# Optimization experiments

Hardware: AMD Instinct MI355X
Metric: run time of the kernel (lower is better)

Reference implementation:

```python
import jax, jax.numpy as jnp
import numpy as np

N, C, E = 10000, 128, 640000  # nodes, channels, edges


def setup_inputs() -> dict:
    key = jax.random.key(0)
    k1, k2, k3, k4 = jax.random.split(key, 4)
    x = jax.random.normal(k1, (N, C), dtype=jnp.float32)
    src = jax.random.randint(k2, (E,), 0, N)  # source node of each edge (neighbor j)
    dst = jax.random.randint(k3, (E,), 0, N)  # destination node (center i)
    # EdgeConv linear: in = 2*C (concat[x_i, x_j - x_i]), out = C
    W = jax.random.normal(k4, (2 * C, C), dtype=jnp.float32) / np.sqrt(2.0 * C)
    b = jnp.zeros((C,), dtype=jnp.float32)
    return {"x": x, "W": W, "b": b, "src": src, "dst": dst}


def reference(x, W, b, src, dst):
    # EdgeConv: h_i = max_{j in N(i)} Linear([x_i, x_j - x_i]); then ReLU
    xi = x[dst]                                   # [E, C] gather center feats
    xj = x[src]                                   # [E, C] gather neighbor feats
    msg = jnp.concatenate([xi, xj - xi], axis=-1) @ W + b   # [E, C]
    agg = jax.ops.segment_max(msg, dst, num_segments=x.shape[0])  # [N, C]
    # nodes with no incoming edges get -inf from segment_max; zero them
    agg = jnp.where(jnp.isfinite(agg), agg, jnp.zeros_like(agg))
    return jax.nn.relu(agg)
```

## Files before the change

### kernel.cpp

```cpp
#include <hip/hip_runtime.h>
#include <cstdint>


#define C_CH 128
#define HBLK 256
#define BSH 4
#define BPAD 640

typedef __attribute__((ext_vector_type(8))) short bf16x8;
typedef __attribute__((ext_vector_type(4))) float f32x4;

static inline size_t align_up(size_t v, size_t a) { return (v + a - 1) & ~(a - 1); }

__device__ inline unsigned f2bf_bits(float f) {
    unsigned u = __builtin_bit_cast(unsigned, f);
    return (u + 0x7FFFu + ((u >> 16) & 1u)) >> 16;
}
__device__ inline unsigned mono_key(unsigned u) {
    return (u & 0x80000000u) ? ~u : (u | 0x80000000u);
}

__global__ __launch_bounds__(256) void gemm_mfma(const float* __restrict__ x,
                                                 const float* __restrict__ W,
                                                 const float* __restrict__ bias,
                                                 float* __restrict__ Aarr,
                                                 unsigned short* __restrict__ Bbf,
                                                 int Nn) {
    __shared__ unsigned short Wh[64][136];
    __shared__ unsigned short Wl[64][136];
    int tid = threadIdx.x;
    int col0 = blockIdx.y * 64;
    bool isA = (col0 < C_CH);
    for (int idx = tid; idx < 64 * 64; idx += 256) {
        int c = idx & 63, k = (idx >> 6) * 2;
        int gc = col0 + c;
        float w0, w1;
        if (isA) {
            w0 = W[k * C_CH + gc] - W[(k + C_CH) * C_CH + gc];
            w1 = W[(k + 1) * C_CH + gc] - W[(k + 1 + C_CH) * C_CH + gc];
        } else {
            int g2 = gc - C_CH;
            w0 = W[(k + C_CH) * C_CH + g2];
            w1 = W[(k + 1 + C_CH) * C_CH + g2];
        }
        unsigned h0 = f2bf_bits(w0), h1 = f2bf_bits(w1);
        float hf0 = __builtin_bit_cast(float, h0 << 16);
        float hf1 = __builtin_bit_cast(float, h1 << 16);
        unsigned l0 = f2bf_bits(w0 - hf0), l1 = f2bf_bits(w1 - hf1);
        *(unsigned*)&Wh[c][k] = h0 | (h1 << 16);
        *(unsigned*)&Wl[c][k] = l0 | (l1 << 16);
    }
    __syncthreads();
    int lane = tid & 63, wv = tid >> 6;
    int r0 = blockIdx.x * 64 + wv * 16;
    int arow = min(r0 + (lane & 15), Nn - 1);
    int kgrp = (lane >> 4) * 8;
    f32x4 acc[4] = {};
#pragma unroll
    for (int kk = 0; kk < 4; ++kk) {
        int k0 = kk * 32 + kgrp;
        const float* xp = &x[(size_t)arow * C_CH + k0];
        float4 v0 = *(const float4*)xp;
        float4 v1 = *(const float4*)(xp + 4);
        float vv[8] = {v0.x, v0.y, v0.z, v0.w, v1.x, v1.y, v1.z, v1.w};
        bf16x8 ah, al;
#pragma unroll
        for (int u = 0; u < 8; ++u) {
            unsigned hb = f2bf_bits(vv[u]);
            float hf = __builtin_bit_cast(float, hb << 16);
            ah[u] = (short)hb;
            al[u] = (short)f2bf_bits(vv[u] - hf);
        }
#pragma unroll
        for (int j = 0; j < 4; ++j) {
            int c = j * 16 + (lane & 15);
            bf16x8 bh = *(const bf16x8*)&Wh[c][k0];
            bf16x8 bl = *(const bf16x8*)&Wl[c][k0];
            acc[j] = __builtin_amdgcn_mfma_f32_16x16x32_bf16(ah, bh, acc[j], 0, 0, 0);
            acc[j] = __builtin_amdgcn_mfma_f32_16x16x32_bf16(al, bh, acc[j], 0, 0, 0);
            acc[j] = __builtin_amdgcn_mfma_f32_16x16x32_bf16(ah, bl, acc[j], 0, 0, 0);
        }
    }
#pragma unroll
    for (int j = 0; j < 4; ++j) {
        int gc = col0 + j * 16 + (lane & 15);
        float badd = isA ? bias[gc] : 0.f;
#pragma unroll
        for (int reg = 0; reg < 4; ++reg) {
            int row = r0 + (lane >> 4) * 4 + reg;
            if (row < Nn) {
                if (isA) Aarr[(size_t)row * C_CH + gc] = acc[j][reg] + badd;
                else     Bbf[(size_t)row * C_CH + (gc - C_CH)] =
                             (unsigned short)f2bf_bits(acc[j][reg]);
            }
        }
    }
}

__global__ __launch_bounds__(256) void hist2_k(const int* __restrict__ dst,
                                               int* __restrict__ T2,
                                               int E_, int NBq, int chunk) {
    __shared__ int cnt[BPAD];
    int tid = threadIdx.x, b = blockIdx.x;
    for (int i = tid; i < BPAD; i += 256) cnt[i] = 0;
    __syncthreads();
    int e0 = b * chunk, e1 = min(e0 + chunk, E_);
    int n4 = (e1 - e0) >> 2;
    const int4* d4p = (const int4*)(dst + e0);
    for (int i = tid; i < n4; i += 256) {
        int4 d = d4p[i];
        atomicAdd(&cnt[d.x >> BSH], 1); atomicAdd(&cnt[d.y >> BSH], 1);
        atomicAdd(&cnt[d.z >> BSH], 1); atomicAdd(&cnt[d.w >> BSH], 1);
    }
    for (int i = e0 + n4 * 4 + tid; i < e1; i += 256) atomicAdd(&cnt[dst[i] >> BSH], 1);
    __syncthreads();
    int* Tb = T2 + (size_t)b * BPAD;
    for (int i = tid; i < NBq; i += 256) Tb[i] = cnt[i];
}

__global__ __launch_bounds__(256) void colscan2_k(int* __restrict__ T2,
                                                  int* __restrict__ deg2, int NBq) {
    int tid = threadIdx.x;
    int lane = tid & 63;
    int q = blockIdx.x * 4 + (tid >> 6);
    if (q >= NBq) return;
    int e[4], p[4];
#pragma unroll
    for (int k = 0; k < 4; ++k) e[k] = T2[(size_t)(lane + 64 * k) * BPAD + q];
    int s = 0;
#pragma unroll
    for (int k = 0; k < 4; ++k) { p[k] = s; s += e[k]; }
    int incl = s;
#pragma unroll
    for (int off = 1; off < 64; off <<= 1) {
        int t = __shfl_up(incl, off);
        if (lane >= off) incl += t;
    }
    int excl = incl - s;
#pragma unroll
    for (int k = 0; k < 4; ++k) T2[(size_t)(lane + 64 * k) * BPAD + q] = excl + p[k];
    if (lane == 63) deg2[q] = incl;
}

__global__ __launch_bounds__(1024) void scan_k(const int* __restrict__ deg,
                                               int* __restrict__ offs, int n) {
    __shared__ int wsum[16];
    const int PER = 16;
    int tid = threadIdx.x;
    int base = tid * PER;
    int s = 0;
#pragma unroll
    for (int k = 0; k < PER; ++k) {
        int idx = base + k;
        s += (idx < n) ? deg[idx] : 0;
    }
    int lane = tid & 63, wid = tid >> 6;
    int pref = s;
#pragma unroll
    for (int off = 1; off < 64; off <<= 1) {
        int t = __shfl_up(pref, off);
        if (lane >= off) pref += t;
    }
    if (lane == 63) wsum[wid] = pref;
    __syncthreads();
    if (tid < 16) {
        int v = wsum[tid];
#pragma unroll
        for (int off = 1; off < 16; off <<= 1) {
            int t = __shfl_up(v, off, 16);
            if (tid >= off) v += t;
        }
        wsum[tid] = v;
    }
    __syncthreads();
    int run = ((wid > 0) ? wsum[wid - 1] : 0) + (pref - s);
#pragma unroll
    for (int k = 0; k < PER; ++k) {
        int idx = base + k;
        int v = (idx < n) ? deg[idx] : 0;
        if (idx < n) offs[idx] = run;
        run += v;
    }
    if (tid == 1023) offs[n] = run;
}

__global__ __launch_bounds__(256) void scatter2_k(const int* __restrict__ src,
                                                  const int* __restrict__ dst,
                                                  const int* __restrict__ T2,
                                                  const int* __restrict__ offs2,
                                                  unsigned* __restrict__ epack,
                                                  int E_, int NBq, int chunk) {
    __shared__ int sbase[BPAD];
    __shared__ int cur[BPAD];
    int tid = threadIdx.x, b = blockIdx.x;
    const int* Tb = T2 + (size_t)b * BPAD;
    for (int i = tid; i < NBq; i += 256) {
        sbase[i] = offs2[i] + Tb[i];
        cur[i] = 0;
    }
    __syncthreads();
    int e0 = b * chunk, e1 = min(e0 + chunk, E_);
    int n4 = (e1 - e0) >> 2;
    const int4* d4p = (const int4*)(dst + e0);
    const int4* s4p = (const int4*)(src + e0);
    const int LM = (1 << BSH) - 1;
    for (int i = tid; i < n4; i += 256) {
        int4 d = d4p[i];
        int4 sv = s4p[i];
        int q, r;
        q = d.x >> BSH; r = atomicAdd(&cur[q], 1);
        epack[sbase[q] + r] = ((unsigned)sv.x << BSH) | (unsigned)(d.x & LM);
        q = d.y >> BSH; r = atomicAdd(&cur[q], 1);
        epack[sbase[q] + r] = ((unsigned)sv.y << BSH) | (unsigned)(d.y & LM);
        q = d.z >> BSH; r = atomicAdd(&cur[q], 1);
        epack[sbase[q] + r] = ((unsigned)sv.z << BSH) | (unsigned)(d.z & LM);
        q = d.w >> BSH; r = atomicAdd(&cur[q], 1);
        epack[sbase[q] + r] = ((unsigned)sv.w << BSH) | (unsigned)(d.w & LM);
    }
    for (int i = e0 + n4 * 4 + tid; i < e1; i += 256) {
        int d = dst[i];
        int q = d >> BSH;
        int r = atomicAdd(&cur[q], 1);
        epack[sbase[q] + r] = ((unsigned)src[i] << BSH) | (unsigned)(d & LM);
    }
}

__global__ __launch_bounds__(512) void bucket_max(const float* __restrict__ Aarr,
                                                  const unsigned short* __restrict__ Bbf,
                                                  const int* __restrict__ offs2,
                                                  const unsigned* __restrict__ epack,
                                                  float* __restrict__ out, int Nn) {
    int q = blockIdx.x;
    int n0 = q << BSH;
    if (n0 >= Nn) return;
    __shared__ unsigned acc[1 << BSH][C_CH];
    int tid = threadIdx.x;
    int nloc = min(1 << BSH, Nn - n0);
    for (int i = tid; i < (1 << BSH) * C_CH; i += 512) ((unsigned*)acc)[i] = 0u;
    __syncthreads();
    int s = offs2[q], e = offs2[q + 1];
    int lane = tid & 63, w = tid >> 6;
    const int LM = (1 << BSH) - 1;
    for (int g0 = s + w * 64; g0 < e; g0 += 512) {
        int idx = g0 + lane;
        unsigned pk = (idx < e) ? epack[idx] : 0u;
        int cnt = min(64, e - g0);
#pragma unroll 4
        for (int j = 0; j < cnt; ++j) {
            unsigned p = __shfl(pk, j);
            const unsigned short* bp = &Bbf[(size_t)(p >> BSH) * C_CH];
            unsigned loc = p & LM;
            unsigned k0 = mono_key(((unsigned)bp[lane]) << 16);
            unsigned k1 = mono_key(((unsigned)bp[lane + 64]) << 16);
            atomicMax(&acc[loc][lane], k0);
            atomicMax(&acc[loc][lane + 64], k1);
        }
    }
    __syncthreads();
    for (int p0 = 0; p0 < nloc; p0 += 4) {
        int li = p0 + (tid >> 7);
        int c = tid & 127;
        if (li < nloc) {
            int row = n0 + li;
            unsigned key = acc[li][c];
            float v = 0.f;
            if (key != 0u) {
                unsigned u = (key & 0x80000000u) ? (key & 0x7FFFFFFFu) : ~key;
                float bmax = __builtin_bit_cast(float, u);
                v = fmaxf(Aarr[(size_t)row * C_CH + c] + bmax, 0.f);
            }
            out[(size_t)row * C_CH + c] = v;
        }
    }
}

extern "C" void kernel_launch(void* const* d_in, const int* in_sizes, int n_in,
                              void* d_out, int out_size, void* d_ws, size_t ws_size,
                              hipStream_t stream) {
    const float* x = (const float*)d_in[0];
    const float* W = (const float*)d_in[1];
    const float* b = (const float*)d_in[2];
    const int* src = (const int*)d_in[3];
    const int* dst = (const int*)d_in[4];
    float* out = (float*)d_out;

    const int N = in_sizes[0] / C_CH;
    const int E = in_sizes[3];
    const int NBq = (N + (1 << BSH) - 1) >> BSH;
    const int chunk = (((E + HBLK - 1) / HBLK) + 3) & ~3;

    char* w = (char*)d_ws;
    float* Aarr = (float*)w;                   w += align_up((size_t)N * C_CH * 4, 256);
    unsigned short* Bbf = (unsigned short*)w;  w += align_up((size_t)N * C_CH * 2, 256);
    int* deg2 = (int*)w;                       w += align_up((size_t)BPAD * 4, 256);
    int* offs2 = (int*)w;                      w += align_up((size_t)(BPAD + 1) * 4, 256);
    int* T2 = (int*)w;                         w += align_up((size_t)HBLK * BPAD * 4, 256);
    unsigned* epack = (unsigned*)w;            w += align_up((size_t)E * 4, 256);

    gemm_mfma<<<dim3((N + 63) / 64, 4), 256, 0, stream>>>(x, W, b, Aarr, Bbf, N);
    hist2_k<<<HBLK, 256, 0, stream>>>(dst, T2, E, NBq, chunk);
    colscan2_k<<<(NBq + 3) / 4, 256, 0, stream>>>(T2, deg2, NBq);
    scan_k<<<1, 1024, 0, stream>>>(deg2, offs2, NBq);
    scatter2_k<<<HBLK, 256, 0, stream>>>(src, dst, T2, offs2, epack, E, NBq, chunk);
    bucket_max<<<NBq, 512, 0, stream>>>(Aarr, Bbf, offs2, epack, out, N);
}
```

Before: 147.9 us.

## Sort bucket edges per node in LDS and reduce max in registers

Replaces the per-edge LDS atomicMax accumulation in bucket_max with a local counting sort of each bucket's packed edges by destination node. Each wave then owns two destination nodes and keeps their channel maxima in registers, using packed 16-bit monotonic keys with an elementwise max over 8 batched gathers. This removes shared-memory atomics and widens the Bbf loads to 32-bit per lane, at the cost of extra sort passes and barriers per 2048-edge chunk.

```diff
diff --git a/kernel.cpp b/kernel.cpp
--- a/kernel.cpp
+++ b/kernel.cpp
@@ -6,18 +6,17 @@
 #define HBLK 256
 #define BSH 4
 #define BPAD 640
+#define SCAP 2048
 
 typedef __attribute__((ext_vector_type(8))) short bf16x8;
 typedef __attribute__((ext_vector_type(4))) float f32x4;
+typedef __attribute__((ext_vector_type(2))) unsigned short u16x2v;
 
 static inline size_t align_up(size_t v, size_t a) { return (v + a - 1) & ~(a - 1); }
 
 __device__ inline unsigned f2bf_bits(float f) {
     unsigned u = __builtin_bit_cast(unsigned, f);
     return (u + 0x7FFFu + ((u >> 16) & 1u)) >> 16;
-}
-__device__ inline unsigned mono_key(unsigned u) {
-    return (u & 0x80000000u) ? ~u : (u | 0x80000000u);
 }
 
 __global__ __launch_bounds__(256) void gemm_mfma(const float* __restrict__ x,
@@ -233,44 +232,82 @@
     int q = blockIdx.x;
     int n0 = q << BSH;
     if (n0 >= Nn) return;
-    __shared__ unsigned acc[1 << BSH][C_CH];
+    __shared__ unsigned sorted[SCAP];
+    __shared__ int cnt[1 << BSH], cbase[1 << BSH], cur[1 << BSH];
     int tid = threadIdx.x;
-    int nloc = min(1 << BSH, Nn - n0);
-    for (int i = tid; i < (1 << BSH) * C_CH; i += 512) ((unsigned*)acc)[i] = 0u;
-    __syncthreads();
-    int s = offs2[q], e = offs2[q + 1];
     int lane = tid & 63, w = tid >> 6;
     const int LM = (1 << BSH) - 1;
-    for (int g0 = s + w * 64; g0 < e; g0 += 512) {
-        int idx = g0 + lane;
-        unsigned pk = (idx < e) ? epack[idx] : 0u;
-        int cnt = min(64, e - g0);
-#pragma unroll 4
-        for (int j = 0; j < cnt; ++j) {
-            unsigned p = __shfl(pk, j);
-            const unsigned short* bp = &Bbf[(size_t)(p >> BSH) * C_CH];
-            unsigned loc = p & LM;
-            unsigned k0 = mono_key(((unsigned)bp[lane]) << 16);
-            unsigned k1 = mono_key(((unsigned)bp[lane + 64]) << 16);
-            atomicMax(&acc[loc][lane], k0);
-            atomicMax(&acc[loc][lane + 64], k1);
-        }
-    }
-    __syncthreads();
-    for (int p0 = 0; p0 < nloc; p0 += 4) {
-        int li = p0 + (tid >> 7);
-        int c = tid & 127;
-        if (li < nloc) {
-            int row = n0 + li;
-            unsigned key = acc[li][c];
-            float v = 0.f;
-            if (key != 0u) {
-                unsigned u = (key & 0x80000000u) ? (key & 0x7FFFFFFFu) : ~key;
-                float bmax = __builtin_bit_cast(float, u);
-                v = fmaxf(Aarr[(size_t)row * C_CH + c] + bmax, 0.f);
+    int s = offs2[q], e = offs2[q + 1];
+
+    unsigned acc0 = 0u, acc1 = 0u;
+    int esum0 = 0, esum1 = 0;
+
+    for (int c0 = s; c0 < e; c0 += SCAP) {
+        int ccnt = min(SCAP, e - c0);
+        if (tid < (1 << BSH)) cnt[tid] = 0;
+        __syncthreads();
+        for (int i = tid; i < ccnt; i += 512) atomicAdd(&cnt[epack[c0 + i] & LM], 1);
+        __syncthreads();
+        if (tid == 0) {
+            int r = 0;
+#pragma unroll
+            for (int k = 0; k < (1 << BSH); ++k) { cbase[k] = r; r += cnt[k]; }
+        }
+        __syncthreads();
+        if (tid < (1 << BSH)) cur[tid] = cbase[tid];
+        __syncthreads();
+        for (int i = tid; i < ccnt; i += 512) {
+            unsigned p = epack[c0 + i];
+            int r = atomicAdd(&cur[p & LM], 1);
+            sorted[r] = p;
+        }
+        __syncthreads();
+#pragma unroll
+        for (int sub = 0; sub < 2; ++sub) {
+            int loc = 2 * w + sub;
+            int ss = cbase[loc], ee = cbase[loc] + cnt[loc];
+            unsigned a = (sub == 0) ? acc0 : acc1;
+            for (int j = ss; j < ee; j += 8) {
+                unsigned wv[8];
+#pragma unroll
+                for (int u = 0; u < 8; ++u) {
+                    int idx = min(j + u, ee - 1);
+                    unsigned row = sorted[idx] >> BSH;
+                    wv[u] = *(const unsigned*)&Bbf[(size_t)row * C_CH + 2 * lane];
+                }
+#pragma unroll
+                for (int u = 0; u < 8; ++u) {
+                    unsigned uu = wv[u];
+                    unsigned sgn = (uu >> 15) & 0x00010001u;
+                    unsigned key = uu ^ (0x80008000u | (sgn * 0x7FFFu));
+                    u16x2v av = __builtin_bit_cast(u16x2v, a);
+                    u16x2v kv = __builtin_bit_cast(u16x2v, key);
+                    a = __builtin_bit_cast(unsigned, __builtin_elementwise_max(av, kv));
+                }
             }
-            out[(size_t)row * C_CH + c] = v;
-        }
+            if (sub == 0) { acc0 = a; esum0 += cnt[loc]; }
+            else          { acc1 = a; esum1 += cnt[loc]; }
+        }
+        __syncthreads();
+    }
+
+#pragma unroll
+    for (int sub = 0; sub < 2; ++sub) {
+        int row = n0 + 2 * w + sub;
+        if (row >= Nn) continue;
+        unsigned a = (sub == 0) ? acc0 : acc1;
+        int es = (sub == 0) ? esum0 : esum1;
+        float2 o = make_float2(0.f, 0.f);
+        if (es > 0) {
+            unsigned t = (a >> 15) & 0x00010001u;
+            unsigned h = a ^ (0xFFFFFFFFu - t * 0x7FFFu);
+            float blo = __builtin_bit_cast(float, (h & 0xFFFFu) << 16);
+            float bhi = __builtin_bit_cast(float, h & 0xFFFF0000u);
+            const float2 av = *(const float2*)&Aarr[(size_t)row * C_CH + 2 * lane];
+            o.x = fmaxf(av.x + blo, 0.f);
+            o.y = fmaxf(av.y + bhi, 0.f);
+        }
+        *(float2*)&out[(size_t)row * C_CH + 2 * lane] = o;
     }
 }
 
```

After: 119.0 us. 19.5% less time.

## Fuse GEMM with histogram, merge scans, use register packed-bf16 max in bucket kernel

Applied to the files above, without the earlier changes.

Merges the GEMM and dst histogram into one launch with block-id dispatch, and folds the column scan and global offset scan into one kernel that uses a last-block-done atomic counter. The bucket max kernel is rewritten to stage edge indices in shared memory and keep per-warp register accumulators. Each lane handles two bf16 channels with packed 16-bit max and a switch on the local node, which replaces shared-memory atomicMax, followed by a cross-warp reduction. This removes launches and LDS atomics, but adds a memset launch, a switch per edge and a threadfence-based completion protocol.

```diff
diff --git a/kernel.cpp b/kernel.cpp
--- a/kernel.cpp
+++ b/kernel.cpp
@@ -6,9 +6,12 @@
 #define HBLK 256
 #define BSH 4
 #define BPAD 640
+#define CHK 2048
 
 typedef __attribute__((ext_vector_type(8))) short bf16x8;
 typedef __attribute__((ext_vector_type(4))) float f32x4;
+typedef __attribute__((ext_vector_type(4))) unsigned int u32x4;
+typedef __attribute__((ext_vector_type(2))) unsigned short u16x2v;
 
 static inline size_t align_up(size_t v, size_t a) { return (v + a - 1) & ~(a - 1); }
 
@@ -16,145 +19,170 @@
     unsigned u = __builtin_bit_cast(unsigned, f);
     return (u + 0x7FFFu + ((u >> 16) & 1u)) >> 16;
 }
-__device__ inline unsigned mono_key(unsigned u) {
-    return (u & 0x80000000u) ? ~u : (u | 0x80000000u);
-}
-
-__global__ __launch_bounds__(256) void gemm_mfma(const float* __restrict__ x,
+__device__ inline unsigned pkmax(unsigned a, unsigned b) {
+    u16x2v av = __builtin_bit_cast(u16x2v, a), bv = __builtin_bit_cast(u16x2v, b);
+    return __builtin_bit_cast(unsigned, __builtin_elementwise_max(av, bv));
+}
+#define CASE_UPD(K) case K: acc[K] = pkmax(acc[K], key); break;
+__device__ inline void upd(unsigned p, unsigned v, unsigned (&acc)[16]) {
+    unsigned sgn = (v >> 15) & 0x00010001u;
+    unsigned key = v ^ (0x80008000u | (sgn * 0x7FFFu));
+    switch (p & 15u) {
+        CASE_UPD(0) CASE_UPD(1) CASE_UPD(2) CASE_UPD(3)
+        CASE_UPD(4) CASE_UPD(5) CASE_UPD(6) CASE_UPD(7)
+        CASE_UPD(8) CASE_UPD(9) CASE_UPD(10) CASE_UPD(11)
+        CASE_UPD(12) CASE_UPD(13) CASE_UPD(14) CASE_UPD(15)
+    }
+}
+
+__global__ __launch_bounds__(256) void gemm_hist(const float* __restrict__ x,
                                                  const float* __restrict__ W,
                                                  const float* __restrict__ bias,
                                                  float* __restrict__ Aarr,
                                                  unsigned short* __restrict__ Bbf,
-                                                 int Nn) {
+                                                 const int* __restrict__ dst,
+                                                 int* __restrict__ T2,
+                                                 int Nn, int E_, int chunk) {
     __shared__ unsigned short Wh[64][136];
     __shared__ unsigned short Wl[64][136];
+    __shared__ int cnt[BPAD];
     int tid = threadIdx.x;
-    int col0 = blockIdx.y * 64;
-    bool isA = (col0 < C_CH);
-    for (int idx = tid; idx < 64 * 64; idx += 256) {
-        int c = idx & 63, k = (idx >> 6) * 2;
-        int gc = col0 + c;
-        float w0, w1;
-        if (isA) {
-            w0 = W[k * C_CH + gc] - W[(k + C_CH) * C_CH + gc];
-            w1 = W[(k + 1) * C_CH + gc] - W[(k + 1 + C_CH) * C_CH + gc];
-        } else {
-            int g2 = gc - C_CH;
-            w0 = W[(k + C_CH) * C_CH + g2];
-            w1 = W[(k + 1 + C_CH) * C_CH + g2];
-        }
-        unsigned h0 = f2bf_bits(w0), h1 = f2bf_bits(w1);
-        float hf0 = __builtin_bit_cast(float, h0 << 16);
-        float hf1 = __builtin_bit_cast(float, h1 << 16);
-        unsigned l0 = f2bf_bits(w0 - hf0), l1 = f2bf_bits(w1 - hf1);
-        *(unsigned*)&Wh[c][k] = h0 | (h1 << 16);
-        *(unsigned*)&Wl[c][k] = l0 | (l1 << 16);
-    }
-    __syncthreads();
-    int lane = tid & 63, wv = tid >> 6;
-    int r0 = blockIdx.x * 64 + wv * 16;
-    int arow = min(r0 + (lane & 15), Nn - 1);
-    int kgrp = (lane >> 4) * 8;
-    f32x4 acc[4] = {};
-#pragma unroll
-    for (int kk = 0; kk < 4; ++kk) {
-        int k0 = kk * 32 + kgrp;
-        const float* xp = &x[(size_t)arow * C_CH + k0];
-        float4 v0 = *(const float4*)xp;
-        float4 v1 = *(const float4*)(xp + 4);
-        float vv[8] = {v0.x, v0.y, v0.z, v0.w, v1.x, v1.y, v1.z, v1.w};
-        bf16x8 ah, al;
-#pragma unroll
-        for (int u = 0; u < 8; ++u) {
-            unsigned hb = f2bf_bits(vv[u]);
-            float hf = __builtin_bit_cast(float, hb << 16);
-            ah[u] = (short)hb;
-            al[u] = (short)f2bf_bits(vv[u] - hf);
+    int GX = (Nn + 63) >> 6;
+    int bid = blockIdx.x;
+    if (bid < GX * 4) {
+        int bx = bid % GX, by = bid / GX;
+        int col0 = by * 64;
+        bool isA = (col0 < C_CH);
+        for (int idx = tid; idx < 64 * 64; idx += 256) {
+            int c = idx & 63, k = (idx >> 6) * 2;
+            int gc = col0 + c;
+            float w0, w1;
+            if (isA) {
+                w0 = W[k * C_CH + gc] - W[(k + C_CH) * C_CH + gc];
+                w1 = W[(k + 1) * C_CH + gc] - W[(k + 1 + C_CH) * C_CH + gc];
+            } else {
+                int g2 = gc - C_CH;
+                w0 = W[(k + C_CH) * C_CH + g2];
+                w1 = W[(k + 1 + C_CH) * C_CH + g2];
+            }
+            unsigned h0 = f2bf_bits(w0), h1 = f2bf_bits(w1);
+            float hf0 = __builtin_bit_cast(float, h0 << 16);
+            float hf1 = __builtin_bit_cast(float, h1 << 16);
+            unsigned l0 = f2bf_bits(w0 - hf0), l1 = f2bf_bits(w1 - hf1);
+            *(unsigned*)&Wh[c][k] = h0 | (h1 << 16);
+            *(unsigned*)&Wl[c][k] = l0 | (l1 << 16);
+        }
+        __syncthreads();
+        int lane = tid & 63, wv = tid >> 6;
+        int r0 = bx * 64 + wv * 16;
+        int arow = min(r0 + (lane & 15), Nn - 1);
+        int kgrp = (lane >> 4) * 8;
+        f32x4 acc[4] = {};
+#pragma unroll
+        for (int kk = 0; kk < 4; ++kk) {
+            int k0 = kk * 32 + kgrp;
+            const float* xp = &x[(size_t)arow * C_CH + k0];
+            float4 v0 = *(const float4*)xp;
+            float4 v1 = *(const float4*)(xp + 4);
+            float vv[8] = {v0.x, v0.y, v0.z, v0.w, v1.x, v1.y, v1.z, v1.w};
+            bf16x8 ah, al;
+#pragma unroll
+            for (int u = 0; u < 8; ++u) {
+                unsigned hb = f2bf_bits(vv[u]);
+                float hf = __builtin_bit_cast(float, hb << 16);
+                ah[u] = (short)hb;
+                al[u] = (short)f2bf_bits(vv[u] - hf);
+            }
+#pragma unroll
+            for (int j = 0; j < 4; ++j) {
+                int c = j * 16 + (lane & 15);
+                bf16x8 bh = *(const bf16x8*)&Wh[c][k0];
+                bf16x8 bl = *(const bf16x8*)&Wl[c][k0];
+                acc[j] = __builtin_amdgcn_mfma_f32_16x16x32_bf16(ah, bh, acc[j], 0, 0, 0);
+                acc[j] = __builtin_amdgcn_mfma_f32_16x16x32_bf16(al, bh, acc[j], 0, 0, 0);
+                acc[j] = __builtin_amdgcn_mfma_f32_16x16x32_bf16(ah, bl, acc[j], 0, 0, 0);
+            }
         }
 #pragma unroll
         for (int j = 0; j < 4; ++j) {
-            int c = j * 16 + (lane & 15);
-            bf16x8 bh = *(const bf16x8*)&Wh[c][k0];
-            bf16x8 bl = *(const bf16x8*)&Wl[c][k0];
-            acc[j] = __builtin_amdgcn_mfma_f32_16x16x32_bf16(ah, bh, acc[j], 0, 0, 0);
-            acc[j] = __builtin_amdgcn_mfma_f32_16x16x32_bf16(al, bh, acc[j], 0, 0, 0);
-            acc[j] = __builtin_amdgcn_mfma_f32_16x16x32_bf16(ah, bl, acc[j], 0, 0, 0);
-        }
-    }
-#pragma unroll
-    for (int j = 0; j < 4; ++j) {
-        int gc = col0 + j * 16 + (lane & 15);
-        float badd = isA ? bias[gc] : 0.f;
-#pragma unroll
-        for (int reg = 0; reg < 4; ++reg) {
-            int row = r0 + (lane >> 4) * 4 + reg;
-            if (row < Nn) {
-                if (isA) Aarr[(size_t)row * C_CH + gc] = acc[j][reg] + badd;
-                else     Bbf[(size_t)row * C_CH + (gc - C_CH)] =
-                             (unsigned short)f2bf_bits(acc[j][reg]);
-            }
-        }
-    }
-}
-
-__global__ __launch_bounds__(256) void hist2_k(const int* __restrict__ dst,
-                                               int* __restrict__ T2,
-                                               int E_, int NBq, int chunk) {
-    __shared__ int cnt[BPAD];
-    int tid = threadIdx.x, b = blockIdx.x;
-    for (int i = tid; i < BPAD; i += 256) cnt[i] = 0;
-    __syncthreads();
-    int e0 = b * chunk, e1 = min(e0 + chunk, E_);
-    int n4 = (e1 - e0) >> 2;
-    const int4* d4p = (const int4*)(dst + e0);
-    for (int i = tid; i < n4; i += 256) {
-        int4 d = d4p[i];
-        atomicAdd(&cnt[d.x >> BSH], 1); atomicAdd(&cnt[d.y >> BSH], 1);
-        atomicAdd(&cnt[d.z >> BSH], 1); atomicAdd(&cnt[d.w >> BSH], 1);
-    }
-    for (int i = e0 + n4 * 4 + tid; i < e1; i += 256) atomicAdd(&cnt[dst[i] >> BSH], 1);
-    __syncthreads();
-    int* Tb = T2 + (size_t)b * BPAD;
-    for (int i = tid; i < NBq; i += 256) Tb[i] = cnt[i];
-}
-
-__global__ __launch_bounds__(256) void colscan2_k(int* __restrict__ T2,
-                                                  int* __restrict__ deg2, int NBq) {
+            int gc = col0 + j * 16 + (lane & 15);
+            float badd = isA ? bias[gc] : 0.f;
+#pragma unroll
+            for (int reg = 0; reg < 4; ++reg) {
+                int row = r0 + (lane >> 4) * 4 + reg;
+                if (row < Nn) {
+                    if (isA) Aarr[(size_t)row * C_CH + gc] = acc[j][reg] + badd;
+                    else     Bbf[(size_t)row * C_CH + (gc - C_CH)] =
+                                 (unsigned short)f2bf_bits(acc[j][reg]);
+                }
+            }
+        }
+    } else {
+        int b = bid - GX * 4;
+        int NBq = (Nn + (1 << BSH) - 1) >> BSH;
+        for (int i = tid; i < BPAD; i += 256) cnt[i] = 0;
+        __syncthreads();
+        int e0 = b * chunk, e1 = min(e0 + chunk, E_);
+        int n4 = (e1 - e0) >> 2;
+        const int4* d4p = (const int4*)(dst + e0);
+        for (int i = tid; i < n4; i += 256) {
+            int4 d = d4p[i];
+            atomicAdd(&cnt[d.x >> BSH], 1); atomicAdd(&cnt[d.y >> BSH], 1);
+            atomicAdd(&cnt[d.z >> BSH], 1); atomicAdd(&cnt[d.w >> BSH], 1);
+        }
+        for (int i = e0 + n4 * 4 + tid; i < e1; i += 256) atomicAdd(&cnt[dst[i] >> BSH], 1);
+        __syncthreads();
+        int* Tb = T2 + (size_t)b * BPAD;
+        for (int i = tid; i < NBq; i += 256) Tb[i] = cnt[i];
+    }
+}
+
+__global__ __launch_bounds__(256) void colscan_scan_k(int* __restrict__ T2,
+                                                      int* __restrict__ deg2,
+                                                      int* __restrict__ offs2,
+                                                      int* __restrict__ done, int NBq) {
+    __shared__ int wsum[4];
+    __shared__ int amLast;
     int tid = threadIdx.x;
     int lane = tid & 63;
     int q = blockIdx.x * 4 + (tid >> 6);
-    if (q >= NBq) return;
-    int e[4], p[4];
-#pragma unroll
-    for (int k = 0; k < 4; ++k) e[k] = T2[(size_t)(lane + 64 * k) * BPAD + q];
-    int s = 0;
-#pragma unroll
-    for (int k = 0; k < 4; ++k) { p[k] = s; s += e[k]; }
-    int incl = s;
-#pragma unroll
-    for (int off = 1; off < 64; off <<= 1) {
-        int t = __shfl_up(incl, off);
-        if (lane >= off) incl += t;
-    }
-    int excl = incl - s;
-#pragma unroll
-    for (int k = 0; k < 4; ++k) T2[(size_t)(lane + 64 * k) * BPAD + q] = excl + p[k];
-    if (lane == 63) deg2[q] = incl;
-}
-
-__global__ __launch_bounds__(1024) void scan_k(const int* __restrict__ deg,
-                                               int* __restrict__ offs, int n) {
-    __shared__ int wsum[16];
-    const int PER = 16;
-    int tid = threadIdx.x;
+    if (q < NBq) {
+        int e[4], p[4];
+#pragma unroll
+        for (int k = 0; k < 4; ++k) e[k] = T2[(size_t)(lane + 64 * k) * BPAD + q];
+        int s = 0;
+#pragma unroll
+        for (int k = 0; k < 4; ++k) { p[k] = s; s += e[k]; }
+        int incl = s;
+#pragma unroll
+        for (int off = 1; off < 64; off <<= 1) {
+            int t = __shfl_up(incl, off);
+            if (lane >= off) incl += t;
+        }
+        int excl = incl - s;
+#pragma unroll
+        for (int k = 0; k < 4; ++k) T2[(size_t)(lane + 64 * k) * BPAD + q] = excl + p[k];
+        if (lane == 63) deg2[q] = incl;
+    }
+    __syncthreads();
+    if (tid == 0) {
+        __threadfence();
+        amLast = (atomicAdd(done, 1) == (int)gridDim.x - 1);
+    }
+    __syncthreads();
+    if (!amLast) return;
+    __threadfence();
+    const int PER = 4;
     int base = tid * PER;
+    int v[PER];
     int s = 0;
 #pragma unroll
     for (int k = 0; k < PER; ++k) {
         int idx = base + k;
-        s += (idx < n) ? deg[idx] : 0;
-    }
-    int lane = tid & 63, wid = tid >> 6;
+        v[k] = (idx < NBq) ? deg2[idx] : 0;
+        s += v[k];
+    }
+    int wid = tid >> 6;
     int pref = s;
 #pragma unroll
     for (int off = 1; off < 64; off <<= 1) {
@@ -163,25 +191,24 @@
     }
     if (lane == 63) wsum[wid] = pref;
     __syncthreads();
-    if (tid < 16) {
-        int v = wsum[tid];
-#pragma unroll
-        for (int off = 1; off < 16; off <<= 1) {
-            int t = __shfl_up(v, off, 16);
-            if (tid >= off) v += t;
-        }
-        wsum[tid] = v;
+    if (tid < 4) {
+        int vv = wsum[tid];
+#pragma unroll
+        for (int off = 1; off < 4; off <<= 1) {
+            int t = __shfl_up(vv, off, 4);
+            if (tid >= off) vv += t;
+        }
+        wsum[tid] = vv;
     }
     __syncthreads();
     int run = ((wid > 0) ? wsum[wid - 1] : 0) + (pref - s);
 #pragma unroll
     for (int k = 0; k < PER; ++k) {
         int idx = base + k;
-        int v = (idx < n) ? deg[idx] : 0;
-        if (idx < n) offs[idx] = run;
-        run += v;
-    }
-    if (tid == 1023) offs[n] = run;
+        if (idx < NBq) offs2[idx] = run;
+        run += v[k];
+    }
+    if (tid == 255) offs2[NBq] = run;
 }
 
 __global__ __launch_bounds__(256) void scatter2_k(const int* __restrict__ src,
@@ -233,43 +260,60 @@
     int q = blockIdx.x;
     int n0 = q << BSH;
     if (n0 >= Nn) return;
-    __shared__ unsigned acc[1 << BSH][C_CH];
+    __shared__ unsigned estage[CHK];
+    __shared__ unsigned macc[8][16][64];
     int tid = threadIdx.x;
-    int nloc = min(1 << BSH, Nn - n0);
-    for (int i = tid; i < (1 << BSH) * C_CH; i += 512) ((unsigned*)acc)[i] = 0u;
-    __syncthreads();
+    int lane = tid & 63, w = tid >> 6;
     int s = offs2[q], e = offs2[q + 1];
-    int lane = tid & 63, w = tid >> 6;
-    const int LM = (1 << BSH) - 1;
-    for (int g0 = s + w * 64; g0 < e; g0 += 512) {
-        int idx = g0 + lane;
-        unsigned pk = (idx < e) ? epack[idx] : 0u;
-        int cnt = min(64, e - g0);
-#pragma unroll 4
-        for (int j = 0; j < cnt; ++j) {
-            unsigned p = __shfl(pk, j);
-            const unsigned short* bp = &Bbf[(size_t)(p >> BSH) * C_CH];
-            unsigned loc = p & LM;
-            unsigned k0 = mono_key(((unsigned)bp[lane]) << 16);
-            unsigned k1 = mono_key(((unsigned)bp[lane + 64]) << 16);
-            atomicMax(&acc[loc][lane], k0);
-            atomicMax(&acc[loc][lane + 64], k1);
-        }
-    }
-    __syncthreads();
-    for (int p0 = 0; p0 < nloc; p0 += 4) {
-        int li = p0 + (tid >> 7);
-        int c = tid & 127;
-        if (li < nloc) {
-            int row = n0 + li;
-            unsigned key = acc[li][c];
-            float v = 0.f;
-            if (key != 0u) {
-                unsigned u = (key & 0x80000000u) ? (key & 0x7FFFFFFFu) : ~key;
-                float bmax = __builtin_bit_cast(float, u);
-                v = fmaxf(Aarr[(size_t)row * C_CH + c] + bmax, 0.f);
-            }
-            out[(size_t)row * C_CH + c] = v;
+
+    unsigned acc[16];
+#pragma unroll
+    for (int k = 0; k < 16; ++k) acc[k] = 0u;
+
+    for (int c0 = s; c0 < e; c0 += CHK) {
+        int ccnt = min(CHK, e - c0);
+        int pad4 = (ccnt + 3) & ~3;
+        for (int i = tid; i < pad4; i += 512)
+            estage[i] = epack[c0 + min(i, ccnt - 1)];
+        __syncthreads();
+        int ng = pad4 >> 2;
+        for (int g = w; g < ng; g += 8) {
+            u32x4 pv = *(const u32x4*)&estage[4 * g];
+            unsigned p0 = __builtin_amdgcn_readfirstlane(pv[0]);
+            unsigned p1 = __builtin_amdgcn_readfirstlane(pv[1]);
+            unsigned p2 = __builtin_amdgcn_readfirstlane(pv[2]);
+            unsigned p3 = __builtin_amdgcn_readfirstlane(pv[3]);
+            unsigned v0 = *(const unsigned*)&Bbf[(size_t)(p0 >> BSH) * C_CH + 2 * lane];
+            unsigned v1 = *(const unsigned*)&Bbf[(size_t)(p1 >> BSH) * C_CH + 2 * lane];
+            unsigned v2 = *(const unsigned*)&Bbf[(size_t)(p2 >> BSH) * C_CH + 2 * lane];
+            unsigned v3 = *(const unsigned*)&Bbf[(size_t)(p3 >> BSH) * C_CH + 2 * lane];
+            upd(p0, v0, acc); upd(p1, v1, acc);
+            upd(p2, v2, acc); upd(p3, v3, acc);
+        }
+        __syncthreads();
+    }
+
+#pragma unroll
+    for (int k = 0; k < 16; ++k) macc[w][k][lane] = acc[k];
+    __syncthreads();
+    for (int sl = tid; sl < 16 * 64; sl += 512) {
+        int loc = sl >> 6, ln = sl & 63;
+        unsigned m = macc[0][loc][ln];
+#pragma unroll
+        for (int ww = 1; ww < 8; ++ww) m = pkmax(m, macc[ww][loc][ln]);
+        int row = n0 + loc;
+        if (row < Nn) {
+            float2 o = make_float2(0.f, 0.f);
+            if (m != 0u) {
+                unsigned t = (m >> 15) & 0x00010001u;
+                unsigned h = m ^ (0xFFFFFFFFu - t * 0x7FFFu);
+                float blo = __builtin_bit_cast(float, (h & 0xFFFFu) << 16);
+                float bhi = __builtin_bit_cast(float, h & 0xFFFF0000u);
+                const float2 av = *(const float2*)&Aarr[(size_t)row * C_CH + 2 * ln];
+                o.x = fmaxf(av.x + blo, 0.f);
+                o.y = fmaxf(av.y + bhi, 0.f);
+            }
+            *(float2*)&out[(size_t)row * C_CH + 2 * ln] = o;
         }
     }
 }
@@ -288,6 +332,7 @@
     const int E = in_sizes[3];
     const int NBq = (N + (1 << BSH) - 1) >> BSH;
     const int chunk = (((E + HBLK - 1) / HBLK) + 3) & ~3;
+    const int GX = (N + 63) >> 6;
 
     char* w = (char*)d_ws;
     float* Aarr = (float*)w;                   w += align_up((size_t)N * C_CH * 4, 256);
@@ -296,11 +341,12 @@
     int* offs2 = (int*)w;                      w += align_up((size_t)(BPAD + 1) * 4, 256);
     int* T2 = (int*)w;                         w += align_up((size_t)HBLK * BPAD * 4, 256);
     unsigned* epack = (unsigned*)w;            w += align_up((size_t)E * 4, 256);
-
-    gemm_mfma<<<dim3((N + 63) / 64, 4), 256, 0, stream>>>(x, W, b, Aarr, Bbf, N);
-    hist2_k<<<HBLK, 256, 0, stream>>>(dst, T2, E, NBq, chunk);
-    colscan2_k<<<(NBq + 3) / 4, 256, 0, stream>>>(T2, deg2, NBq);
-    scan_k<<<1, 1024, 0, stream>>>(deg2, offs2, NBq);
+    int* done = (int*)w;                       w += 256;
+
+    hipMemsetAsync(done, 0, 4, stream);
+
+    gemm_hist<<<GX * 4 + HBLK, 256, 0, stream>>>(x, W, b, Aarr, Bbf, dst, T2, N, E, chunk);
+    colscan_scan_k<<<(NBq + 3) / 4, 256, 0, stream>>>(T2, deg2, offs2, done, NBq);
     scatter2_k<<<HBLK, 256, 0, stream>>>(src, dst, T2, offs2, epack, E, NBq, chunk);
     bucket_max<<<NBq, 512, 0, stream>>>(Aarr, Bbf, offs2, epack, out, N);
 }
```

New measurement: 160.5 us. +8.6%, slower.
